# Kernel tuning notes

Measured on AMD Instinct MI355X. Metric: run time of the kernel, lower is better.

The kernel has to match this reference:

```python
import jax, jax.numpy as jnp
import numpy as np

B, E, C = 16384, 8, 10        # batch, n_experts, n_contexts
IN, H1, H2 = 39, 1024, 1024   # obs dim, backbone widths
HH, OUT = 512, 4              # head hidden, action dim


def _xavier(key, shape):
    fan_in, fan_out = shape[-2], shape[-1]
    scale = jnp.sqrt(2.0 / (fan_in + fan_out)).astype(jnp.float32)
    return jax.random.normal(key, shape, jnp.float32) * scale


def setup_inputs() -> dict:
    key = jax.random.key(0)
    ks = jax.random.split(key, 12)
    return {
        "state": jax.random.normal(ks[0], (B, IN), jnp.float32),
        "c": jax.random.randint(ks[1], (B,), 0, C, jnp.int32),
        "W_te": _xavier(ks[2], (E, C)),            # task encoder (torch Linear weight [out,in])
        "Wb1": _xavier(ks[3], (E, IN, H1)),        # per-expert backbone layer 1
        "bb1": jnp.zeros((E, H1), jnp.float32),
        "Wb2": _xavier(ks[4], (E, H1, H2)),        # per-expert backbone layer 2
        "bb2": jnp.zeros((E, H2), jnp.float32),
        "Wh1": _xavier(ks[5], (C, H2, HH)),        # per-context head layer
        "bh1": jnp.zeros((C, HH), jnp.float32),
        "Wh2": _xavier(ks[6], (C, HH, OUT)),       # per-context output layer
        "bh2": jnp.zeros((C, OUT), jnp.float32),
    }


def reference(state, c, W_te, Wb1, bb1, Wb2, bb2, Wh1, bh1, Wh2, bh2):
    # Mixture weights: one_hot(c) @ W_te.T  ==  gather columns of W_te.
    w = W_te[:, c].T                                                   # [B, E]
    # Parallel expert backbone (InputLayer + ParallelLayer): ReLU MLP per expert.
    h = jax.nn.relu(jnp.einsum('bi,eio->ebo', state, Wb1) + bb1[:, None, :])   # [E, B, H1]
    feat = jax.nn.relu(jnp.einsum('ebh,eho->ebo', h, Wb2) + bb2[:, None, :])   # [E, B, H2]
    feat = jax.nn.relu(feat)                                           # agg_activation[0] (idempotent)
    # Soft mixture combine: w[B,1,E] @ feat_perm[B,E,H2] -> [B,H2]
    f = jax.nn.relu(jnp.einsum('be,ebh->bh', w, feat))                 # agg_activation[1]
    # Per-context head dispatch: compute all C heads, gather each sample's context.
    y1 = jax.nn.relu(jnp.einsum('bh,chj->bcj', f, Wh1) + bh1[None])    # [B, C, HH]
    y1 = jnp.take_along_axis(y1, c[:, None, None].astype(jnp.int32), axis=1)[:, 0]  # [B, HH]
    y2 = jnp.einsum('bj,cjo->bco', y1, Wh2) + bh2[None]                # [B, C, OUT]
    a = jnp.take_along_axis(y2, c[:, None, None].astype(jnp.int32), axis=1)[:, 0]   # [B, OUT]
    return a
```

## Files before the change

### kernel.cpp

```cpp
#include <hip/hip_runtime.h>
#include <stdint.h>

#define DEVI __device__ __forceinline__

typedef float f32x4 __attribute__((ext_vector_type(4)));
typedef short bf16x8 __attribute__((ext_vector_type(8)));

constexpr int Bq  = 16384;
constexpr int Eq  = 8;
constexpr int Cq  = 10;
constexpr int INq = 39;
constexpr int INP = 64;
constexpr int H1q = 1024;
constexpr int H2q = 1024;
constexpr int HHq = 512;
constexpr int OUTq = 4;

DEVI unsigned short bf16_rne(float x){
  unsigned u = __builtin_bit_cast(unsigned, x);
  u += 0x7FFFu + ((u >> 16) & 1u);
  return (unsigned short)(u >> 16);
}

DEVI void dma16(const unsigned short* g, unsigned short* l){
  __builtin_amdgcn_global_load_lds(
      (const __attribute__((address_space(1))) unsigned int*)g,
      (__attribute__((address_space(3))) unsigned int*)l,
      16, 0, 0);
}

DEVI void mfma_step1(const unsigned short* lsb, int lane, int wm, int wn, f32x4 acc[4][4]){
  const int g = lane >> 4;
  bf16x8 a[4], b[4];
#pragma unroll
  for (int mf = 0; mf < 4; ++mf){
    int r = wm*64 + mf*16 + (lane & 15);
    a[mf] = *(const bf16x8*)(lsb + r*32 + (g ^ ((r >> 1) & 3))*8);
  }
#pragma unroll
  for (int nf = 0; nf < 4; ++nf){
    int r = wn*64 + nf*16 + (lane & 15);
    b[nf] = *(const bf16x8*)(lsb + 4096 + r*32 + (g ^ ((r >> 1) & 3))*8);
  }
#pragma unroll
  for (int nf = 0; nf < 4; ++nf)
#pragma unroll
    for (int mf = 0; mf < 4; ++mf)
      acc[mf][nf] = __builtin_amdgcn_mfma_f32_16x16x32_bf16(a[mf], b[nf], acc[mf][nf], 0, 0, 0);
}

__global__ void k_tcast(const float* __restrict__ src, unsigned short* __restrict__ dst,
                        int R, int Cc, int Rpad){
  __shared__ float t[32][33];
  const int z = blockIdx.z;
  const int c0 = blockIdx.x*32, r0 = blockIdx.y*32;
  const float* s = src + (size_t)z*R*Cc;
#pragma unroll
  for (int i = 0; i < 4; ++i){
    int r = r0 + threadIdx.y + i*8;
    int cc = c0 + threadIdx.x;
    float v = (r < R && cc < Cc) ? s[(size_t)r*Cc + cc] : 0.f;
    t[threadIdx.y + i*8][threadIdx.x] = v;
  }
  __syncthreads();
  const size_t dbase = (size_t)z*Cc*Rpad;
#pragma unroll
  for (int i = 0; i < 4; ++i){
    int cc = c0 + threadIdx.y + i*8;
    int r  = r0 + threadIdx.x;
    if (cc < Cc && r < Rpad)
      dst[dbase + (size_t)cc*Rpad + r] = bf16_rne(t[threadIdx.x][threadIdx.y + i*8]);
  }
}

__global__ void k_scast(const float* __restrict__ st, unsigned short* __restrict__ sB){
  int i = blockIdx.x*blockDim.x + threadIdx.x;
  if (i >= Bq*INP) return;
  int b = i >> 6, kk = i & 63;
  sB[i] = bf16_rne((kk < INq) ? st[b*INq + kk] : 0.f);
}

__global__ void k_bucket(const int* __restrict__ c, int b0, int Bc,
                         int* __restrict__ cnt, int* __restrict__ poff,
                         int* __restrict__ perm){
  __shared__ int lcnt[Cq];
  __shared__ int lcur[Cq];
  const int tid = threadIdx.x;
  if (tid < Cq) lcnt[tid] = 0;
  __syncthreads();
  for (int i = tid; i < Bc; i += blockDim.x) atomicAdd(&lcnt[c[b0 + i]], 1);
  __syncthreads();
  if (tid == 0){
    int s = 0;
    for (int k = 0; k < Cq; ++k){ poff[k] = s; lcur[k] = s; cnt[k] = lcnt[k]; s += lcnt[k]; }
  }
  __syncthreads();
  for (int i = tid; i < Bc; i += blockDim.x){
    int p = atomicAdd(&lcur[c[b0 + i]], 1);
    perm[p] = i;
  }
}

__global__ __launch_bounds__(256, 2)
void k_h(const unsigned short* __restrict__ sB, const unsigned short* __restrict__ w1B,
         const float* __restrict__ bb1, unsigned short* __restrict__ hB,
         int e0, int b0, int Bc){
  __shared__ unsigned short ls[2][2][4096];
  const int tid = threadIdx.x, lane = tid & 63, wid = tid >> 6;
  const int wm = wid >> 1, wn = wid & 1;
  const int bt = blockIdx.x, ot = blockIdx.y, el = blockIdx.z;
  const int ge = e0 + el;
  const int rl = lane >> 2, cs = lane & 3;
  const int corig = cs ^ ((rl >> 1) & 3);

  const f32x4 vz = {0.f, 0.f, 0.f, 0.f};
  f32x4 acc[4][4];
#pragma unroll
  for (int a = 0; a < 4; ++a)
#pragma unroll
    for (int b = 0; b < 4; ++b) acc[a][b] = vz;

  auto stage = [&](int buf, int s){
    const int k0 = s*32;
    const int half = wid & 1;
    if (wid < 2){
#pragma unroll
      for (int i = 0; i < 4; ++i){
        int seg = half*4 + i;
        int r = b0 + bt*128 + seg*16 + rl;
        dma16(sB + (size_t)r*INP + k0 + corig*8, &ls[buf][0][0] + seg*512);
      }
    } else {
#pragma unroll
      for (int i = 0; i < 4; ++i){
        int seg = half*4 + i;
        int r = ge*H1q + ot*128 + seg*16 + rl;
        dma16(w1B + (size_t)r*INP + k0 + corig*8, &ls[buf][1][0] + seg*512);
      }
    }
  };

  stage(0, 0);
  for (int s = 0; s < 2; ++s){
    __syncthreads();
    if (s == 0) stage(1, 1);
    mfma_step1(&ls[s][0][0], lane, wm, wn, acc);
  }

  const int rbase = bt*128 + wm*64 + 4*(lane >> 4);
  const int cbase = ot*128 + wn*64 + (lane & 15);
#pragma unroll
  for (int nf = 0; nf < 4; ++nf){
    const int col = cbase + nf*16;
    const float bias = bb1[ge*H1q + col];
#pragma unroll
    for (int mf = 0; mf < 4; ++mf){
#pragma unroll
      for (int j = 0; j < 4; ++j){
        int row = rbase + mf*16 + j;
        hB[((size_t)el*Bc + row)*H1q + col] = bf16_rne(fmaxf(acc[mf][nf][j] + bias, 0.f));
      }
    }
  }
}

__global__ __launch_bounds__(256, 2)
void k_moe(const unsigned short* __restrict__ hB, const unsigned short* __restrict__ w2B,
           const float* __restrict__ Wte, const int* __restrict__ cIn,
           const float* __restrict__ bb2, float* __restrict__ f32f,
           unsigned short* __restrict__ fB,
           int e0, int G, int first, int last, int b0, int Bc){
  __shared__ unsigned short ls[2][2][4096];
  __shared__ float lWte[Eq*Cq];
  const int tid = threadIdx.x, lane = tid & 63, wid = tid >> 6;
  const int wm = wid >> 1, wn = wid & 1;
  const int bt = blockIdx.x, ot = blockIdx.y;
  if (tid < Eq*Cq) lWte[tid] = Wte[tid];

  const int rl = lane >> 2, cs = lane & 3;
  const int corig = cs ^ ((rl >> 1) & 3);
  const int rbase = bt*128 + wm*64 + 4*(lane >> 4);
  const int cbase = ot*128 + wn*64 + (lane & 15);

  int cidx[16];
#pragma unroll
  for (int mf = 0; mf < 4; ++mf)
#pragma unroll
    for (int j = 0; j < 4; ++j)
      cidx[mf*4 + j] = cIn[b0 + rbase + mf*16 + j];

  const f32x4 vz = {0.f, 0.f, 0.f, 0.f};
  f32x4 acc[4][4], facc[4][4];
#pragma unroll
  for (int a = 0; a < 4; ++a)
#pragma unroll
    for (int b = 0; b < 4; ++b){ acc[a][b] = vz; facc[a][b] = vz; }

  if (!first){
#pragma unroll
    for (int mf = 0; mf < 4; ++mf)
#pragma unroll
      for (int nf = 0; nf < 4; ++nf)
#pragma unroll
        for (int j = 0; j < 4; ++j)
          facc[mf][nf][j] = f32f[(size_t)(rbase + mf*16 + j)*H2q + cbase + nf*16];
  }

  auto stage = [&](int buf, int s){
    const int el = s >> 5;
    const int k0 = (s & 31)*32;
    const int half = wid & 1;
    if (wid < 2){
#pragma unroll
      for (int i = 0; i < 4; ++i){
        int seg = half*4 + i;
        int r = bt*128 + seg*16 + rl;
        dma16(hB + ((size_t)el*Bc + r)*H1q + k0 + corig*8, &ls[buf][0][0] + seg*512);
      }
    } else {
#pragma unroll
      for (int i = 0; i < 4; ++i){
        int seg = half*4 + i;
        int r = el*H2q + ot*128 + seg*16 + rl;
        dma16(w2B + (size_t)r*H1q + k0 + corig*8, &ls[buf][1][0] + seg*512);
      }
    }
  };

  const int total = G*32;
  stage(0, 0);
  for (int s = 0; s < total; ++s){
    __syncthreads();
    if (s + 1 < total) stage((s + 1) & 1, s + 1);
    mfma_step1(&ls[s & 1][0][0], lane, wm, wn, acc);
    if ((s & 31) == 31){
      const int ge = e0 + (s >> 5);
#pragma unroll
      for (int nf = 0; nf < 4; ++nf){
        const float bias = bb2[ge*H2q + cbase + nf*16];
#pragma unroll
        for (int mf = 0; mf < 4; ++mf){
          f32x4 v = acc[mf][nf];
          acc[mf][nf] = vz;
#pragma unroll
          for (int j = 0; j < 4; ++j){
            float w = lWte[ge*Cq + cidx[mf*4 + j]];
            facc[mf][nf][j] += w * fmaxf(v[j] + bias, 0.f);
          }
        }
      }
    }
  }

#pragma unroll
  for (int mf = 0; mf < 4; ++mf)
#pragma unroll
    for (int nf = 0; nf < 4; ++nf)
#pragma unroll
      for (int j = 0; j < 4; ++j){
        const size_t o = (size_t)(rbase + mf*16 + j)*H2q + cbase + nf*16;
        if (last) fB[o] = bf16_rne(fmaxf(facc[mf][nf][j], 0.f));
        else      f32f[o] = facc[mf][nf][j];
      }
}

__global__ __launch_bounds__(256, 2)
void k_head1(const unsigned short* __restrict__ fB, const unsigned short* __restrict__ whB,
             const float* __restrict__ bh1,
             const int* __restrict__ perm, const int* __restrict__ cnt,
             const int* __restrict__ poff, float* __restrict__ y1p){
  __shared__ unsigned short ls[2][2][4096];
  const int tile = blockIdx.x, ct = blockIdx.y, ot = blockIdx.z;
  const int n = cnt[ct];
  const int rem = n - tile*128;
  if (rem <= 0) return;
  const int tid = threadIdx.x, lane = tid & 63, wid = tid >> 6;
  const int wm = wid >> 1, wn = wid & 1;
  const int rl = lane >> 2, cs = lane & 3;
  const int corig = cs ^ ((rl >> 1) & 3);
  const int base = poff[ct] + tile*128;

  int prow[4];
#pragma unroll
  for (int i = 0; i < 4; ++i){
    int seg = (wid & 1)*4 + i;
    int lr = seg*16 + rl;
    prow[i] = perm[base + (lr < rem ? lr : 0)];
  }

  const f32x4 vz = {0.f, 0.f, 0.f, 0.f};
  f32x4 acc[4][4];
#pragma unroll
  for (int a = 0; a < 4; ++a)
#pragma unroll
    for (int b = 0; b < 4; ++b) acc[a][b] = vz;

  auto stage = [&](int buf, int s){
    const int k0 = s*32;
    const int half = wid & 1;
    if (wid < 2){
#pragma unroll
      for (int i = 0; i < 4; ++i){
        int seg = half*4 + i;
        dma16(fB + (size_t)prow[i]*H2q + k0 + corig*8, &ls[buf][0][0] + seg*512);
      }
    } else {
#pragma unroll
      for (int i = 0; i < 4; ++i){
        int seg = half*4 + i;
        int r = ct*HHq + ot*128 + seg*16 + rl;
        dma16(whB + (size_t)r*H2q + k0 + corig*8, &ls[buf][1][0] + seg*512);
      }
    }
  };

  stage(0, 0);
  for (int s = 0; s < 32; ++s){
    __syncthreads();
    if (s + 1 < 32) stage((s + 1) & 1, s + 1);
    mfma_step1(&ls[s & 1][0][0], lane, wm, wn, acc);
  }

  const int rloc = wm*64 + 4*(lane >> 4);
  const int cbase = ot*128 + wn*64 + (lane & 15);
#pragma unroll
  for (int nf = 0; nf < 4; ++nf){
    const int col = cbase + nf*16;
    const float bias = bh1[ct*HHq + col];
#pragma unroll
    for (int mf = 0; mf < 4; ++mf){
#pragma unroll
      for (int j = 0; j < 4; ++j){
        int lr = rloc + mf*16 + j;
        if (lr < rem)
          y1p[(size_t)(base + lr)*HHq + col] = fmaxf(acc[mf][nf][j] + bias, 0.f);
      }
    }
  }
}

__global__ void k_head2(const float* __restrict__ y1p, const float* __restrict__ Wh2,
                        const float* __restrict__ bh2, const int* __restrict__ perm,
                        const int* __restrict__ cIn, float* __restrict__ out, int b0){
  const int tid = threadIdx.x, lane = tid & 63, w = tid >> 6;
  const int pos = blockIdx.x*4 + w;
  const int orig = b0 + perm[pos];
  const int ct = cIn[orig];
  const float* yrow = y1p + (size_t)pos*HHq;
  const float* wct  = Wh2 + (size_t)ct*HHq*OUTq;
  f32x4 s = {0.f, 0.f, 0.f, 0.f};
  const int kb = lane*8;
  f32x4 y0 = *(const f32x4*)(yrow + kb);
  f32x4 y1 = *(const f32x4*)(yrow + kb + 4);
#pragma unroll
  for (int t = 0; t < 4; ++t){
    f32x4 wv = *(const f32x4*)(wct + (size_t)(kb + t)*4);
    s += y0[t]*wv;
  }
#pragma unroll
  for (int t = 0; t < 4; ++t){
    f32x4 wv = *(const f32x4*)(wct + (size_t)(kb + 4 + t)*4);
    s += y1[t]*wv;
  }
#pragma unroll
  for (int o = 0; o < 4; ++o){
    float v = s[o];
#pragma unroll
    for (int d = 32; d > 0; d >>= 1) v += __shfl_xor(v, d);
    if (lane == 0) out[(size_t)orig*OUTq + o] = v + bh2[ct*OUTq + o];
  }
}

extern "C" void kernel_launch(void* const* d_in, const int* in_sizes, int n_in,
                              void* d_out, int out_size, void* d_ws, size_t ws_size,
                              hipStream_t stream){
  (void)in_sizes; (void)n_in; (void)out_size;
  const float* state = (const float*)d_in[0];
  const int*   cVec  = (const int*)  d_in[1];
  const float* Wte   = (const float*)d_in[2];
  const float* Wb1   = (const float*)d_in[3];
  const float* bb1   = (const float*)d_in[4];
  const float* Wb2   = (const float*)d_in[5];
  const float* bb2   = (const float*)d_in[6];
  const float* Wh1   = (const float*)d_in[7];
  const float* bh1   = (const float*)d_in[8];
  const float* Wh2   = (const float*)d_in[9];
  const float* bh2   = (const float*)d_in[10];
  float* out = (float*)d_out;

  auto A = [](size_t x) -> size_t { return (x + 255) & ~(size_t)255; };
  auto mx = [](size_t a, size_t b) -> size_t { return a > b ? a : b; };

  const size_t pers = A((size_t)Bq*INP*2)
                    + A((size_t)Eq*H1q*INP*2)
                    + A((size_t)Cq*HHq*H2q*2)
                    + A((size_t)Bq*4) + 2*A(64);

  const int candNB[8] = {1, 1, 1, 1, 2, 4, 8, 16};
  const int candG [8] = {8, 4, 2, 1, 1, 1, 1, 1};
  int NB = 16, G = 1;
  for (int i = 0; i < 8; ++i){
    size_t Bc = (size_t)Bq / candNB[i];
    int g = candG[i];
    size_t need = pers
                + A((size_t)g*H2q*H1q*2)
                + mx(A((size_t)g*Bc*H1q*2), A(Bc*(size_t)HHq*4))
                + A(Bc*(size_t)H2q*2)
                + (g < 8 ? A(Bc*(size_t)H2q*4) : 0);
    if (need <= ws_size){ NB = candNB[i]; G = candG[i]; break; }
  }
  const int Bc = Bq / NB;

  char* ws = (char*)d_ws;
  size_t p = 0;
  auto alloc = [&](size_t bytes) -> void* { void* r = ws + p; p += A(bytes); return r; };

  unsigned short* sB  = (unsigned short*)alloc((size_t)Bq*INP*2);
  unsigned short* w1B = (unsigned short*)alloc((size_t)Eq*H1q*INP*2);
  unsigned short* whB = (unsigned short*)alloc((size_t)Cq*HHq*H2q*2);
  int* perm = (int*)alloc((size_t)Bq*4);
  int* cnt  = (int*)alloc(64);
  int* poff = (int*)alloc(64);
  unsigned short* w2B = (unsigned short*)alloc((size_t)G*H2q*H1q*2);
  char* r1 = (char*)alloc(mx(A((size_t)G*Bc*H1q*2), A((size_t)Bc*HHq*4)));
  unsigned short* hB = (unsigned short*)r1;
  float* y1p = (float*)r1;
  unsigned short* fB = (unsigned short*)alloc((size_t)Bc*H2q*2);
  float* f32f = (G < 8) ? (float*)alloc((size_t)Bc*H2q*4) : (float*)fB;

  const dim3 tb(32, 8, 1);
  k_tcast<<<dim3(16, 32, 10), tb, 0, stream>>>(Wh1, whB, H2q, HHq, H2q);
  k_tcast<<<dim3(32, 2, 8), tb, 0, stream>>>(Wb1, w1B, INq, H1q, INP);
  k_scast<<<(Bq*INP + 255)/256, 256, 0, stream>>>(state, sB);

  const int nch = Eq / G;
  for (int nb = 0; nb < NB; ++nb){
    const int b0 = nb*Bc;
    k_bucket<<<1, 1024, 0, stream>>>(cVec, b0, Bc, cnt, poff, perm);
    for (int ec = 0; ec < nch; ++ec){
      const int e0 = ec*G;
      k_tcast<<<dim3(32, 32, G), tb, 0, stream>>>(Wb2 + (size_t)e0*H1q*H2q, w2B,
                                                  H1q, H2q, H1q);
      k_h  <<<dim3(Bc/128, 8, G), 256, 0, stream>>>(sB, w1B, bb1, hB, e0, b0, Bc);
      k_moe<<<dim3(Bc/128, 8), 256, 0, stream>>>(hB, w2B, Wte, cVec, bb2, f32f, fB,
                                                 e0, G, ec == 0 ? 1 : 0,
                                                 ec == nch - 1 ? 1 : 0, b0, Bc);
    }
    k_head1<<<dim3(Bc/128, 10, 4), 256, 0, stream>>>(fB, whB, bh1, perm, cnt, poff, y1p);
    k_head2<<<Bc/4, 256, 0, stream>>>(y1p, Wh2, bh2, perm, cVec, out, b0);
  }
}
```

Baseline: 702.1 us.

## Triple-buffer k_moe LDS pipeline and prefer all-expert chunks with hoisted Wb2 cast

The k_moe main loop moves from a double buffer to a three-stage LDS ring. Loads are issued two steps ahead, and raw s_waitcnt vmcnt plus s_barrier replace __syncthreads, so global loads overlap more of the MFMA work. The expert-2 bias is cached in shared memory as bf16 instead of being read from global memory at each expert boundary. Host-side selection now prefers processing all 8 experts at once by splitting the batch, with the Wb2 transpose-cast hoisted out of the batch loop when G==8. Risks include the larger LDS footprint lowering occupancy, fragile manual wait counts, and a small precision loss from rounding the bias to bf16.

```diff
diff --git a/kernel.cpp b/kernel.cpp
--- a/kernel.cpp
+++ b/kernel.cpp
@@ -20,6 +20,10 @@
   unsigned u = __builtin_bit_cast(unsigned, x);
   u += 0x7FFFu + ((u >> 16) & 1u);
   return (unsigned short)(u >> 16);
+}
+DEVI float bf16f(unsigned short h){
+  unsigned u = ((unsigned)h) << 16;
+  return __builtin_bit_cast(float, u);
 }
 
 DEVI void dma16(const unsigned short* g, unsigned short* l){
@@ -170,17 +174,22 @@
            const float* __restrict__ bb2, float* __restrict__ f32f,
            unsigned short* __restrict__ fB,
            int e0, int G, int first, int last, int b0, int Bc){
-  __shared__ unsigned short ls[2][2][4096];
+  __shared__ unsigned short ls[3][2][4096];
   __shared__ float lWte[Eq*Cq];
+  __shared__ unsigned short lbb2[Eq*128];
   const int tid = threadIdx.x, lane = tid & 63, wid = tid >> 6;
   const int wm = wid >> 1, wn = wid & 1;
   const int bt = blockIdx.x, ot = blockIdx.y;
+
   if (tid < Eq*Cq) lWte[tid] = Wte[tid];
+  for (int i = tid; i < G*128; i += 256)
+    lbb2[i] = bf16_rne(bb2[(size_t)(e0 + (i >> 7))*H2q + ot*128 + (i & 127)]);
 
   const int rl = lane >> 2, cs = lane & 3;
   const int corig = cs ^ ((rl >> 1) & 3);
   const int rbase = bt*128 + wm*64 + 4*(lane >> 4);
   const int cbase = ot*128 + wn*64 + (lane & 15);
+  const int cloc  = wn*64 + (lane & 15);
 
   int cidx[16];
 #pragma unroll
@@ -229,15 +238,23 @@
 
   const int total = G*32;
   stage(0, 0);
+  stage(1, 1);
+  asm volatile("s_waitcnt vmcnt(4) lgkmcnt(0)" ::: "memory");
+  asm volatile("s_barrier" ::: "memory");
+
+  int cur = 0;
   for (int s = 0; s < total; ++s){
-    __syncthreads();
-    if (s + 1 < total) stage((s + 1) & 1, s + 1);
-    mfma_step1(&ls[s & 1][0][0], lane, wm, wn, acc);
+    if (s + 2 < total){
+      int b2 = cur + 2; if (b2 >= 3) b2 -= 3;
+      stage(b2, s + 2);
+    }
+    mfma_step1(&ls[cur][0][0], lane, wm, wn, acc);
     if ((s & 31) == 31){
       const int ge = e0 + (s >> 5);
+      const int el = s >> 5;
 #pragma unroll
       for (int nf = 0; nf < 4; ++nf){
-        const float bias = bb2[ge*H2q + cbase + nf*16];
+        const float bias = bf16f(lbb2[el*128 + cloc + nf*16]);
 #pragma unroll
         for (int mf = 0; mf < 4; ++mf){
           f32x4 v = acc[mf][nf];
@@ -250,6 +267,10 @@
         }
       }
     }
+    if (s + 2 < total) asm volatile("s_waitcnt vmcnt(4)" ::: "memory");
+    else               asm volatile("s_waitcnt vmcnt(0)" ::: "memory");
+    asm volatile("s_barrier" ::: "memory");
+    cur = (cur + 1 == 3) ? 0 : cur + 1;
   }
 
 #pragma unroll
@@ -396,10 +417,10 @@
                     + A((size_t)Cq*HHq*H2q*2)
                     + A((size_t)Bq*4) + 2*A(64);
 
-  const int candNB[8] = {1, 1, 1, 1, 2, 4, 8, 16};
-  const int candG [8] = {8, 4, 2, 1, 1, 1, 1, 1};
+  const int candNB[9] = {1, 2, 4, 8, 16, 16, 16, 16, 16};
+  const int candG [9] = {8, 8, 8, 8, 16==16?8:8, 4, 2, 1, 1};
   int NB = 16, G = 1;
-  for (int i = 0; i < 8; ++i){
+  for (int i = 0; i < 9; ++i){
     size_t Bc = (size_t)Bq / candNB[i];
     int g = candG[i];
     size_t need = pers
@@ -407,7 +428,7 @@
                 + mx(A((size_t)g*Bc*H1q*2), A(Bc*(size_t)HHq*4))
                 + A(Bc*(size_t)H2q*2)
                 + (g < 8 ? A(Bc*(size_t)H2q*4) : 0);
-    if (need <= ws_size){ NB = candNB[i]; G = candG[i]; break; }
+    if (need <= ws_size){ NB = candNB[i]; G = g; break; }
   }
   const int Bc = Bq / NB;
 
@@ -432,6 +453,8 @@
   k_tcast<<<dim3(16, 32, 10), tb, 0, stream>>>(Wh1, whB, H2q, HHq, H2q);
   k_tcast<<<dim3(32, 2, 8), tb, 0, stream>>>(Wb1, w1B, INq, H1q, INP);
   k_scast<<<(Bq*INP + 255)/256, 256, 0, stream>>>(state, sB);
+  if (G == Eq)
+    k_tcast<<<dim3(32, 32, Eq), tb, 0, stream>>>(Wb2, w2B, H1q, H2q, H1q);
 
   const int nch = Eq / G;
   for (int nb = 0; nb < NB; ++nb){
@@ -439,8 +462,9 @@
     k_bucket<<<1, 1024, 0, stream>>>(cVec, b0, Bc, cnt, poff, perm);
     for (int ec = 0; ec < nch; ++ec){
       const int e0 = ec*G;
-      k_tcast<<<dim3(32, 32, G), tb, 0, stream>>>(Wb2 + (size_t)e0*H1q*H2q, w2B,
-                                                  H1q, H2q, H1q);
+      if (G < Eq)
+        k_tcast<<<dim3(32, 32, G), tb, 0, stream>>>(Wb2 + (size_t)e0*H1q*H2q, w2B,
+                                                    H1q, H2q, H1q);
       k_h  <<<dim3(Bc/128, 8, G), 256, 0, stream>>>(sB, w1B, bb1, hB, e0, b0, Bc);
       k_moe<<<dim3(Bc/128, 8), 256, 0, stream>>>(hB, w2B, Wte, cVec, bb2, f32f, fB,
                                                  e0, G, ec == 0 ? 1 : 0,
```

New measurement: 693.1 us. About the same (-1.3%).
